# Optimization experiments

Hardware: AMD Instinct MI355X
Metric: run time of the kernel (lower is better)

The kernel has to match this reference:

```python
import math
import jax, jax.numpy as jnp
from jax import lax
import numpy as np

C = 19
SIZE = 33
MIOU = [0.95, 0.78, 0.88, 0.45, 0.48, 0.55, 0.6, 0.7, 0.9, 0.58, 0.92,
        0.75, 0.5, 0.91, 0.62, 0.7, 0.55, 0.42, 0.68]


def _class_weights(mious):
    mious = np.asarray(mious, dtype=np.float64)
    ratios = 1.0 / (mious / (mious.sum() + 1e-6) + 1e-6)
    r_max, r_min = ratios.max(), ratios.min()
    w = (ratios - r_min + 1e-6) / (r_max - r_min + 1e-6)
    return jnp.asarray(w, dtype=jnp.float32)


def setup_inputs() -> dict:
    key = jax.random.key(0)
    logit = jax.random.normal(key, (1, C, 1024, 2048), dtype=jnp.float32)
    return {"logit": logit, "class_weights": _class_weights(MIOU)}


def reference(logit, class_weights):
    x = logit[0]                                   # [C, H, W]
    p = jax.nn.softmax(x, axis=0)                  # [C, H, W]
    predict = jnp.argmax(p, axis=0)                # [H, W] int
    one_hot = jax.nn.one_hot(predict, C, dtype=jnp.float32)   # [H, W, C]
    one_hot = jnp.transpose(one_hot, (2, 0, 1))[None]          # [1, C, H, W]

    # 33x33 box filter, depthwise (groups=C), zero padding 16 (SAME)
    k_dw = jnp.ones((C, 1, SIZE, SIZE), dtype=jnp.float32)
    summary = lax.conv_general_dilated(one_hot, k_dw, (1, 1), 'SAME',
                                       feature_group_count=C)   # [1,C,H,W]
    count = jnp.sum(summary, axis=1, keepdims=True)              # [1,1,H,W]
    dist = summary / count
    region_impurity = jnp.sum(-dist * jnp.log(dist + 1e-6), axis=1,
                              keepdims=True) / math.log(19)      # [1,1,H,W]

    pixel_entropy = jnp.sum(-p * jnp.log(p + 1e-6), axis=0)       # [H, W]
    # per-pixel class-indexed weight gather (replaces the CPU loop)
    wt_pixel_entropy = pixel_entropy * class_weights[predict]     # [H, W]
    wt_pixel_entropy = wt_pixel_entropy[None, None] / math.log(19)

    k1 = jnp.ones((1, 1, SIZE, SIZE), dtype=jnp.float32)
    region_sum_entropy = lax.conv_general_dilated(wt_pixel_entropy, k1,
                                                  (1, 1), 'SAME')
    prediction_uncertainty = region_sum_entropy / count
    score = region_impurity * prediction_uncertainty
    return (score[0, 0], region_impurity[0, 0], prediction_uncertainty[0, 0])
```

## Files before the change

kernel.cpp:

```cpp
#include <hip/hip_runtime.h>
#include <stdint.h>

#define HH 1024
#define WW 2048
#define HWC (HH * WW)
#define NC 19
#define RAD 16
static constexpr float INV_LN19 = 1.0f / 2.9444389791664403f;

static __device__ __forceinline__ int imin(int a, int b) { return a < b ? a : b; }
static __device__ __forceinline__ int imax(int a, int b) { return a > b ? a : b; }

__global__ __launch_bounds__(256) void k1_pix(const float* __restrict__ logit,
                                              const float* __restrict__ cw,
                                              uint8_t* __restrict__ predict,
                                              float* __restrict__ wtent) {
    int t = blockIdx.x * 256 + threadIdx.x;
    int p0 = t * 4;
    float xx[4][NC];
#pragma unroll
    for (int c = 0; c < NC; ++c) {
        float4 v = *reinterpret_cast<const float4*>(logit + (size_t)c * HWC + p0);
        xx[0][c] = v.x; xx[1][c] = v.y; xx[2][c] = v.z; xx[3][c] = v.w;
    }
    float went[4];
    int ids[4];
#pragma unroll
    for (int e = 0; e < 4; ++e) {
        float m = xx[e][0]; int id = 0;
#pragma unroll
        for (int c = 1; c < NC; ++c) { if (xx[e][c] > m) { m = xx[e][c]; id = c; } }
        float s = 0.f, u = 0.f;
#pragma unroll
        for (int c = 0; c < NC; ++c) {
            float d = xx[e][c] - m;
            float ex = __expf(d);
            s += ex;
            u = fmaf(ex, d, u);
        }
        float ent = __logf(s) - u / s;
        went[e] = ent * cw[id] * INV_LN19;
        ids[e] = id;
    }
    uint32_t packed = (uint32_t)ids[0] | ((uint32_t)ids[1] << 8) |
                      ((uint32_t)ids[2] << 16) | ((uint32_t)ids[3] << 24);
    *reinterpret_cast<uint32_t*>(predict + p0) = packed;
    *reinterpret_cast<float4*>(wtent + p0) = make_float4(went[0], went[1], went[2], went[3]);
}

#define TR 32
#define TC 128
#define IR 64
#define IC 160
__global__ __launch_bounds__(256) void k23_fused(const uint8_t* __restrict__ predict,
                                                 const float* __restrict__ wtent,
                                                 float* __restrict__ out) {
    __shared__ __align__(16) char smem[51712];
    uint8_t*  sp8  = reinterpret_cast<uint8_t*>(smem);
    uint32_t* sp32 = reinterpret_cast<uint32_t*>(smem);
    float*    swt  = reinterpret_cast<float*>(smem + 10240);
    float*    sce  = swt;
    uint32_t* scnt = reinterpret_cast<uint32_t*>(smem + 30720);

    int tid = threadIdx.x;
    int r0 = blockIdx.y * TR;
    int w0 = blockIdx.x * TC;

#pragma unroll
    for (int i = 0; i < 10; ++i) {
        int k = tid + i * 256;
        int rr = k / 40, cc = k - rr * 40;
        int grow = r0 - RAD + rr;
        int gcb = w0 - RAD + cc * 4;
        uint32_t v = 0xFFFFFFFFu;
        if ((unsigned)grow < HH && (unsigned)gcb < WW)
            v = *reinterpret_cast<const uint32_t*>(predict + (size_t)grow * WW + gcb);
        sp32[rr * 40 + cc] = v;
    }
#pragma unroll
    for (int i = 0; i < 40; ++i) {
        int k = tid + i * 256;
        int rr = k / 160, cc = k - rr * 160;
        int grow = r0 - RAD + rr;
        int gc = w0 - RAD + cc;
        float v = 0.f;
        if ((unsigned)grow < HH && (unsigned)gc < WW)
            v = wtent[(size_t)grow * WW + gc];
        swt[rr * 160 + cc] = v;
    }
    __syncthreads();

    if (tid < IC) {
        float es = 0.f;
#pragma unroll
        for (int h = 0; h < 32; ++h) es += swt[h * 160 + tid];
        for (int rr = 0; rr < 32; ++rr) {
            float tmp = swt[rr * 160 + tid];
            es += swt[(rr + 32) * 160 + tid];
            sce[rr * 160 + tid] = es;
            es -= tmp;
        }
    }

    int row = tid >> 3;
    int seg = tid & 7;
    int c0 = seg * 16;
    int r = r0 + row;
    float nh = (float)(imin(r + RAD, HH - 1) - imax(r - RAD, 0) + 1);
    float rcpN[16], imp[16];
#pragma unroll
    for (int j = 0; j < 16; ++j) {
        int wc = w0 + c0 + j;
        float nw = (float)(imin(wc + RAD, WW - 1) - imax(wc - RAD, 0) + 1);
        rcpN[j] = 1.0f / (nh * nw);
        imp[j] = 0.f;
    }

    for (int c = 0; c < NC; ++c) {
        __syncthreads();
        if (tid < IC) {
            int cnt = 0;
#pragma unroll
            for (int h = 0; h < 32; ++h) cnt += (sp8[h * 160 + tid] == c);
            for (int rr = 0; rr < 32; ++rr) {
                cnt += (sp8[(rr + 32) * 160 + tid] == c);
                scnt[rr * 164 + tid] = (uint32_t)cnt;
                cnt -= (sp8[rr * 160 + tid] == c);
            }
        }
        __syncthreads();
        const uint32_t* base = scnt + row * 164 + c0;
        int run = 0;
#pragma unroll
        for (int k = 0; k < 32; ++k) run += (int)base[k];
#pragma unroll
        for (int j = 0; j < 16; ++j) {
            int n = run + (int)base[j + 32];
            float dist = (float)n * rcpN[j];
            imp[j] = fmaf(dist, __logf(dist + 1e-6f), imp[j]);
            run = n - (int)base[j];
        }
    }

    const float* ep = sce + row * 160 + c0;
    float erun = 0.f;
#pragma unroll
    for (int k = 0; k < 32; ++k) erun += ep[k];
#pragma unroll
    for (int j = 0; j < 16; ++j) {
        float esum = erun + ep[j + 32];
        float unc = esum * rcpN[j];
        float rim = imp[j] * (-INV_LN19);
        int wc = w0 + c0 + j;
        size_t o = (size_t)r * WW + wc;
        out[o] = rim * unc;
        out[HWC + o] = rim;
        out[2 * HWC + o] = unc;
        erun = esum - ep[j];
    }
}

extern "C" void kernel_launch(void* const* d_in, const int* in_sizes, int n_in,
                              void* d_out, int out_size, void* d_ws, size_t ws_size,
                              hipStream_t stream) {
    const float* logit = (const float*)d_in[0];
    const float* cw = (const float*)d_in[1];
    float* out = (float*)d_out;
    uint8_t* ws = (uint8_t*)d_ws;

    uint8_t* predict = ws;
    float* wtent = (float*)(ws + 2097152);

    k1_pix<<<2048, 256, 0, stream>>>(logit, cw, predict, wtent);
    k23_fused<<<dim3(WW / TC, HH / TR), 256, 0, stream>>>(predict, wtent, out);
}
```

Measured before the change: 315.8 us.

## Pack four class counts per word and stage coalesced output writes via LDS

The k23 kernel now counts four classes at once by packing 8-bit per-class counts into 32-bit words and summing them with SWAR masks. This cuts the class loop from 19 passes to 5. Predictions are loaded straight into registers per column, and vertical entropy sums are read directly from global memory instead of being staged through shared memory. Output values are written to shared memory and stored with a row-major coalesced pattern, with the thread-to-row mapping changed and LDS padded to 165 to avoid bank conflicts. This adds register pressure and uses uncoalesced byte loads for predictions.

After: 286.7 us. 1.1x faster.

```diff
diff --git a/kernel.cpp b/kernel.cpp
--- a/kernel.cpp
+++ b/kernel.cpp
@@ -6,6 +6,10 @@
 #define HWC (HH * WW)
 #define NC 19
 #define RAD 16
+#define TR 32
+#define TC 128
+#define IC 160
+#define SN 165
 static constexpr float INV_LN19 = 1.0f / 2.9444389791664403f;
 
 static __device__ __forceinline__ int imin(int a, int b) { return a < b ? a : b; }
@@ -48,62 +52,54 @@
     *reinterpret_cast<float4*>(wtent + p0) = make_float4(went[0], went[1], went[2], went[3]);
 }
 
-#define TR 32
-#define TC 128
-#define IR 64
-#define IC 160
 __global__ __launch_bounds__(256) void k23_fused(const uint8_t* __restrict__ predict,
                                                  const float* __restrict__ wtent,
                                                  float* __restrict__ out) {
-    __shared__ __align__(16) char smem[51712];
-    uint8_t*  sp8  = reinterpret_cast<uint8_t*>(smem);
-    uint32_t* sp32 = reinterpret_cast<uint32_t*>(smem);
-    float*    swt  = reinterpret_cast<float*>(smem + 10240);
-    float*    sce  = swt;
-    uint32_t* scnt = reinterpret_cast<uint32_t*>(smem + 30720);
+    __shared__ uint32_t s_cnt[TR * SN];
+    __shared__ float    s_ce[TR * SN];
+    const uint32_t M = 0x00FF00FFu;
 
     int tid = threadIdx.x;
     int r0 = blockIdx.y * TR;
     int w0 = blockIdx.x * TC;
 
-#pragma unroll
-    for (int i = 0; i < 10; ++i) {
-        int k = tid + i * 256;
-        int rr = k / 40, cc = k - rr * 40;
-        int grow = r0 - RAD + rr;
-        int gcb = w0 - RAD + cc * 4;
-        uint32_t v = 0xFFFFFFFFu;
-        if ((unsigned)grow < HH && (unsigned)gcb < WW)
-            v = *reinterpret_cast<const uint32_t*>(predict + (size_t)grow * WW + gcb);
-        sp32[rr * 40 + cc] = v;
-    }
-#pragma unroll
-    for (int i = 0; i < 40; ++i) {
-        int k = tid + i * 256;
-        int rr = k / 160, cc = k - rr * 160;
-        int grow = r0 - RAD + rr;
-        int gc = w0 - RAD + cc;
-        float v = 0.f;
-        if ((unsigned)grow < HH && (unsigned)gc < WW)
-            v = wtent[(size_t)grow * WW + gc];
-        swt[rr * 160 + cc] = v;
-    }
-    __syncthreads();
-
+    uint32_t colreg[16];
+    int w = w0 - RAD + tid;
+    bool wok = (tid < IC) && ((unsigned)w < WW);
+    int wcl = wok ? w : 0;
     if (tid < IC) {
+#pragma unroll
+        for (int g = 0; g < 16; ++g) {
+            uint32_t acc = 0;
+#pragma unroll
+            for (int b = 0; b < 4; ++b) {
+                int grow = r0 - RAD + 4 * g + b;
+                bool rok = (unsigned)grow < HH;
+                uint32_t pin = (uint32_t)predict[(size_t)(rok ? grow : 0) * WW + wcl];
+                if (!(rok && wok)) pin = 255u;
+                acc |= pin << (8 * b);
+            }
+            colreg[g] = acc;
+        }
+        const float* wp = wtent + wcl;
         float es = 0.f;
 #pragma unroll
-        for (int h = 0; h < 32; ++h) es += swt[h * 160 + tid];
+        for (int h = 0; h < 32; ++h) {
+            int grow = r0 - RAD + h;
+            if (wok && (unsigned)grow < HH) es += wp[(size_t)grow * WW];
+        }
+#pragma unroll
         for (int rr = 0; rr < 32; ++rr) {
-            float tmp = swt[rr * 160 + tid];
-            es += swt[(rr + 32) * 160 + tid];
-            sce[rr * 160 + tid] = es;
-            es -= tmp;
-        }
-    }
-
-    int row = tid >> 3;
-    int seg = tid & 7;
+            int ga = r0 + RAD + rr;
+            if (wok && (unsigned)ga < HH) es += wp[(size_t)ga * WW];
+            s_ce[rr * SN + tid] = es;
+            int gs = r0 - RAD + rr;
+            if (wok && (unsigned)gs < HH) es -= wp[(size_t)gs * WW];
+        }
+    }
+
+    int row = tid & 31;
+    int seg = tid >> 5;
     int c0 = seg * 16;
     int r = r0 + row;
     float nh = (float)(imin(r + RAD, HH - 1) - imax(r - RAD, 0) + 1);
@@ -116,47 +112,95 @@
         imp[j] = 0.f;
     }
 
-    for (int c = 0; c < NC; ++c) {
+    for (int p = 0; p < 5; ++p) {
         __syncthreads();
         if (tid < IC) {
-            int cnt = 0;
-#pragma unroll
-            for (int h = 0; h < 32; ++h) cnt += (sp8[h * 160 + tid] == c);
+            uint32_t m[32];
+            uint32_t cnt = 0;
+#pragma unroll
+            for (int h = 0; h < 32; ++h) {
+                uint32_t pin = (colreg[h >> 2] >> ((h & 3) * 8)) & 255u;
+                uint32_t mm = ((int)(pin >> 2) == p) ? (1u << ((pin & 3u) << 3)) : 0u;
+                m[h] = mm;
+                cnt += mm;
+            }
+#pragma unroll
             for (int rr = 0; rr < 32; ++rr) {
-                cnt += (sp8[(rr + 32) * 160 + tid] == c);
-                scnt[rr * 164 + tid] = (uint32_t)cnt;
-                cnt -= (sp8[rr * 160 + tid] == c);
+                int h = rr + 32;
+                uint32_t pin = (colreg[h >> 2] >> ((h & 3) * 8)) & 255u;
+                uint32_t mm = ((int)(pin >> 2) == p) ? (1u << ((pin & 3u) << 3)) : 0u;
+                cnt += mm;
+                s_cnt[rr * SN + tid] = cnt;
+                cnt -= m[rr];
             }
         }
         __syncthreads();
-        const uint32_t* base = scnt + row * 164 + c0;
-        int run = 0;
-#pragma unroll
-        for (int k = 0; k < 32; ++k) run += (int)base[k];
+        const uint32_t* base = s_cnt + row * SN + c0;
+        uint32_t cache[16];
+        uint32_t lo = 0, hi = 0;
+#pragma unroll
+        for (int k = 0; k < 32; ++k) {
+            uint32_t v = base[k];
+            if (k < 16) cache[k] = v;
+            lo += v & M;
+            hi += (v >> 8) & M;
+        }
 #pragma unroll
         for (int j = 0; j < 16; ++j) {
-            int n = run + (int)base[j + 32];
-            float dist = (float)n * rcpN[j];
-            imp[j] = fmaf(dist, __logf(dist + 1e-6f), imp[j]);
-            run = n - (int)base[j];
-        }
-    }
-
-    const float* ep = sce + row * 160 + c0;
+            uint32_t vin = base[j + 32];
+            uint32_t nlo = lo + (vin & M);
+            uint32_t nhi = hi + ((vin >> 8) & M);
+            float n0 = (float)(nlo & 0xFFFFu);
+            float n1 = (float)(nhi & 0xFFFFu);
+            float n2 = (float)(nlo >> 16);
+            float n3 = (float)(nhi >> 16);
+            float d0 = n0 * rcpN[j], d1 = n1 * rcpN[j];
+            float d2 = n2 * rcpN[j], d3 = n3 * rcpN[j];
+            imp[j] = fmaf(d0, __logf(d0 + 1e-6f), imp[j]);
+            imp[j] = fmaf(d1, __logf(d1 + 1e-6f), imp[j]);
+            imp[j] = fmaf(d2, __logf(d2 + 1e-6f), imp[j]);
+            imp[j] = fmaf(d3, __logf(d3 + 1e-6f), imp[j]);
+            uint32_t vo = cache[j];
+            lo = nlo - (vo & M);
+            hi = nhi - ((vo >> 8) & M);
+        }
+    }
+
+    const float* ep = s_ce + row * SN + c0;
+    float ecache[16];
     float erun = 0.f;
 #pragma unroll
-    for (int k = 0; k < 32; ++k) erun += ep[k];
+    for (int k = 0; k < 32; ++k) {
+        float v = ep[k];
+        if (k < 16) ecache[k] = v;
+        erun += v;
+    }
+    float unc[16];
 #pragma unroll
     for (int j = 0; j < 16; ++j) {
         float esum = erun + ep[j + 32];
-        float unc = esum * rcpN[j];
-        float rim = imp[j] * (-INV_LN19);
-        int wc = w0 + c0 + j;
-        size_t o = (size_t)r * WW + wc;
-        out[o] = rim * unc;
+        unc[j] = esum * rcpN[j];
+        erun = esum - ecache[j];
+    }
+    __syncthreads();
+
+    float* rimp = reinterpret_cast<float*>(s_cnt);
+#pragma unroll
+    for (int j = 0; j < 16; ++j) {
+        rimp[row * SN + c0 + j] = imp[j] * (-INV_LN19);
+        s_ce[row * SN + c0 + j] = unc[j];
+    }
+    __syncthreads();
+#pragma unroll
+    for (int i = 0; i < 16; ++i) {
+        int idx = tid + 256 * i;
+        int rr = idx >> 7, cc = idx & 127;
+        float rim = rimp[rr * SN + cc];
+        float un = s_ce[rr * SN + cc];
+        size_t o = (size_t)(r0 + rr) * WW + (w0 + cc);
+        out[o] = rim * un;
         out[HWC + o] = rim;
-        out[2 * HWC + o] = unc;
-        erun = esum - ep[j];
+        out[2 * HWC + o] = un;
     }
 }
 
```
